# Optimization experiments

Measured on AMD Instinct MI355X. Metric: run time of the kernel, lower is better.

Reference implementation:

```python
import jax, jax.numpy as jnp
import numpy as np

EPS = 1e-5

def _conv1x1(x, w, b):
    # x: [B, Din, N], w: [Dout, Din], b: [Dout]
    return jnp.einsum('od,bdn->bon', w, x) + b[None, :, None]

def _layernorm_last(x):
    # LayerNorm over last axis, no affine (matches torch LayerNorm([N], elementwise_affine=False))
    mu = jnp.mean(x, axis=-1, keepdims=True)
    var = jnp.mean(jnp.square(x - mu), axis=-1, keepdims=True)
    return (x - mu) * jax.lax.rsqrt(var + EPS)

def setup_inputs() -> dict:
    key = jax.random.key(0)
    ks = jax.random.split(key, 16)
    B, D, N, M = 1, 64, 64 * 80, 4096
    H2 = 2 * D
    s = 0.05
    return {
        'fea_pixel': jax.random.normal(ks[0], (B, D, N), jnp.float32),
        'fea_keypoint': jax.random.normal(ks[1], (B, D, M), jnp.float32),
        'Wq': jax.random.normal(ks[2], (D, D), jnp.float32) * s,
        'bq': jax.random.normal(ks[3], (D,), jnp.float32) * s,
        'Wk': jax.random.normal(ks[4], (D, D), jnp.float32) * s,
        'bk': jax.random.normal(ks[5], (D,), jnp.float32) * s,
        'Wv': jax.random.normal(ks[6], (D, D), jnp.float32) * s,
        'bv': jax.random.normal(ks[7], (D,), jnp.float32) * s,
        'Wm': jax.random.normal(ks[8], (D, D), jnp.float32) * s,
        'bm': jax.random.normal(ks[9], (D,), jnp.float32) * s,
        'W1': jax.random.normal(ks[10], (H2, D), jnp.float32) * s,
        'b1': jax.random.normal(ks[11], (H2,), jnp.float32) * s,
        'W2': jax.random.normal(ks[12], (D, H2), jnp.float32) * s,
        'b2': jax.random.normal(ks[13], (D,), jnp.float32) * s,
    }

def reference(fea_pixel, fea_keypoint, Wq, bq, Wk, bk, Wv, bv, Wm, bm, W1, b1, W2, b2):
    B, D, N = fea_pixel.shape
    num_heads = 4
    hd = D // num_heads  # head dim

    # QKV 1x1-conv projections, then split channels as (head_dim, num_heads) -- matches torch view
    q = _conv1x1(fea_pixel, Wq, bq).reshape(B, hd, num_heads, N)
    k = _conv1x1(fea_keypoint, Wk, bk).reshape(B, hd, num_heads, -1)
    v = _conv1x1(fea_keypoint, Wv, bv).reshape(B, hd, num_heads, -1)

    scores = jnp.einsum('bdhn,bdhm->bhnm', q, k) / jnp.sqrt(jnp.float32(hd))
    prob = jax.nn.softmax(scores, axis=-1)
    x = jnp.einsum('bhnm,bdhm->bdhn', prob, v)  # [B, hd, H, N]
    attn = _conv1x1(x.reshape(B, D, N), Wm, bm)

    fea = _layernorm_last(fea_pixel + attn)  # [B, D, N]

    # MLP over channel dim: operate on [B, N, D]
    y = jnp.swapaxes(fea, 1, 2)
    h = jax.nn.relu(jnp.einsum('bnd,od->bno', y, W1) + b1)
    m = jax.nn.relu(jnp.einsum('bno,do->bnd', h, W2) + b2)

    return _layernorm_last(fea + jnp.swapaxes(m, 1, 2))
```

## Files before the change

### kernel.cpp

```cpp
#include <hip/hip_runtime.h>
#include <hip/hip_bf16.h>

typedef __attribute__((ext_vector_type(4))) short short4v;
typedef __attribute__((ext_vector_type(4))) float float4v;

#define NHEADS 4
#define DMODEL 64
#define EPSV 1e-5f
#define QSCALE 0.36067376022224085f

__device__ inline short bf16rn(float f) {
    __hip_bfloat16 h = __float2bfloat16(f);
    return __builtin_bit_cast(short, h);
}

__device__ inline float exp2fast(float x) { return __builtin_amdgcn_exp2f(x); }

__global__ __launch_bounds__(256)
void proj_all_k(const float* __restrict__ Wk, const float* __restrict__ bk,
                const float* __restrict__ Wv, const float* __restrict__ bv,
                const float* __restrict__ Wq, const float* __restrict__ bq,
                const float* __restrict__ fkey, const float* __restrict__ fpix,
                short4v* __restrict__ kfrag, short4v* __restrict__ vfrag,
                short4v* __restrict__ qfrag, int M, int N) {
    __shared__ float xs[64][64];
    __shared__ float wsm[64][65];
    const int t = threadIdx.x;
    const int kvblocks = M >> 6;
    const bool isKV = (int)blockIdx.x < kvblocks;
    const int c0 = (isKV ? blockIdx.x : blockIdx.x - kvblocks) * 64;
    const float* x = isKV ? fkey : fpix;
    const int NC = isKV ? M : N;

    for (int i = t; i < 64 * 64; i += 256) {
        xs[i >> 6][i & 63] = x[(size_t)(i >> 6) * NC + c0 + (i & 63)];
        if (isKV) wsm[i >> 6][i & 63] = Wv[i];
    }
    __syncthreads();
    const int CT = NC >> 4;

    {
        const float* W = isKV ? Wk : Wq;
        const float* b = isKV ? bk : bq;
        const float scale = isKV ? 1.f : QSCALE;
        short4v* outf = isKV ? kfrag : qfrag;
        const int mm = t & 63;
        const int qd = __builtin_amdgcn_readfirstlane(t >> 6);
        const int m = c0 + mm;
        float acc[16];
        #pragma unroll
        for (int cc = 0; cc < 16; ++cc) acc[cc] = b[qd * 16 + cc];
        #pragma unroll 8
        for (int d = 0; d < 64; ++d) {
            float xv = xs[d][mm];
            #pragma unroll
            for (int cc = 0; cc < 16; ++cc)
                acc[cc] = fmaf(W[(qd * 16 + cc) * 64 + d], xv, acc[cc]);
        }
        #pragma unroll
        for (int h = 0; h < 4; ++h) {
            short4v pk;
            #pragma unroll
            for (int j = 0; j < 4; ++j) pk[j] = bf16rn(acc[j * 4 + h] * scale);
            outf[((size_t)(h * CT + (m >> 4))) * 64 + (m & 15) + 16 * qd] = pk;
        }
    }
    if (isKV) {
        const int lane = t & 63;
        const int w = t >> 6;
        const int d = lane >> 2, h = lane & 3;
        const float b0 = bv[lane];
        #pragma unroll
        for (int r = 0; r < 4; ++r) {
            const int mg = r * 4 + w;
            float a0 = b0, a1 = b0, a2 = b0, a3 = b0;
            #pragma unroll 8
            for (int dd = 0; dd < 64; ++dd) {
                float wv = wsm[lane][dd];
                float4 xv = *(const float4*)&xs[dd][mg * 4];
                a0 = fmaf(wv, xv.x, a0); a1 = fmaf(wv, xv.y, a1);
                a2 = fmaf(wv, xv.z, a2); a3 = fmaf(wv, xv.w, a3);
            }
            short4v pk;
            pk[0] = bf16rn(a0); pk[1] = bf16rn(a1); pk[2] = bf16rn(a2); pk[3] = bf16rn(a3);
            const int m0 = c0 + mg * 4;
            vfrag[((size_t)(h * CT + (m0 >> 4))) * 64 + d + 16 * ((m0 >> 2) & 3)] = pk;
        }
    }
}

__global__ __launch_bounds__(256)
void attn_mfma_k(const short4v* __restrict__ qf, const short4v* __restrict__ kf,
                 const short4v* __restrict__ vf, float* __restrict__ xatt,
                 int N, int M) {
    const int lane = threadIdx.x & 63;
    const int ck = threadIdx.x >> 6;
    const int nt = blockIdx.x;
    const int h = blockIdx.y;
    const int NT = N >> 4, MT = M >> 4;
    const int mtN = MT >> 2;
    const int mt0 = ck * mtN;

    const short4v q4 = qf[((size_t)(h * NT + nt)) * 64 + lane];
    const float4v zero4 = {0.f, 0.f, 0.f, 0.f};
    float4v O = zero4;
    float ld = 0.f;
    const int g4 = (lane >> 4) << 2;

    const short4v* kp = kf + ((size_t)(h * MT + mt0)) * 64 + lane;
    const short4v* vp = vf + ((size_t)(h * MT + mt0)) * 64 + lane;
    for (int it = 0; it < mtN; it += 4) {
        short4v ka[4], va[4];
        #pragma unroll
        for (int u = 0; u < 4; ++u) {
            ka[u] = kp[(it + u) * 64];
            va[u] = vp[(it + u) * 64];
        }
        #pragma unroll
        for (int u = 0; u < 4; ++u) {
            float4v s = __builtin_amdgcn_mfma_f32_16x16x16bf16_1k(ka[u], q4, zero4, 0, 0, 0);
            float p0 = exp2fast(s[0]), p1 = exp2fast(s[1]),
                  p2 = exp2fast(s[2]), p3 = exp2fast(s[3]);
            ld += (p0 + p1) + (p2 + p3);
            short4v pa;
            pa[0] = bf16rn(p0); pa[1] = bf16rn(p1); pa[2] = bf16rn(p2); pa[3] = bf16rn(p3);
            O = __builtin_amdgcn_mfma_f32_16x16x16bf16_1k(pa, va[u], O, 0, 0, 0);
        }
    }
    ld += __shfl_xor(ld, 16);
    ld += __shfl_xor(ld, 32);

    __shared__ float Osm[4][256];
    __shared__ float lsm[4][16];
    #pragma unroll
    for (int b = 0; b < 4; ++b)
        Osm[ck][(g4 + b) * 16 + (lane & 15)] = O[b];
    if (lane < 16) lsm[ck][lane] = ld;
    __syncthreads();

    const int t = threadIdx.x;
    const int d = t >> 4, q = t & 15;
    const float L = (lsm[0][q] + lsm[1][q]) + (lsm[2][q] + lsm[3][q]);
    const int oi = q * 16 + d;
    const float val = (Osm[0][oi] + Osm[1][oi]) + (Osm[2][oi] + Osm[3][oi]);
    xatt[(size_t)(d * NHEADS + h) * N + nt * 16 + q] = val / L;
}

template<int DIN, int DOUT, bool RELU>
__global__ __launch_bounds__(256)
void conv1x1_k(const float* __restrict__ W, const float* __restrict__ bias,
               const float* __restrict__ x, float* __restrict__ out, int N) {
    __shared__ float xs[DIN][64];
    const int tid = threadIdx.x;
    const int n0 = blockIdx.x * 64;
    for (int i = tid; i < DIN * 64; i += 256) {
        int d = i >> 6, nn = i & 63;
        xs[d][nn] = x[(size_t)d * N + n0 + nn];
    }
    __syncthreads();
    const int nn = tid & 63;
    const int og = __builtin_amdgcn_readfirstlane((int)(threadIdx.x >> 6));
    const int ow = blockIdx.y * 16 + og * 4;
    float acc[4];
    #pragma unroll
    for (int i = 0; i < 4; ++i) acc[i] = bias[ow + i];
    #pragma unroll 8
    for (int d = 0; d < DIN; ++d) {
        float xv = xs[d][nn];
        #pragma unroll
        for (int i = 0; i < 4; ++i)
            acc[i] = fmaf(W[(ow + i) * DIN + d], xv, acc[i]);
    }
    #pragma unroll
    for (int i = 0; i < 4; ++i) {
        float r = RELU ? fmaxf(acc[i], 0.f) : acc[i];
        out[(size_t)(ow + i) * N + n0 + nn] = r;
    }
}

__global__ __launch_bounds__(512)
void add_ln_k(const float* __restrict__ a, const float* __restrict__ b,
              float* __restrict__ out, int N) {
    const int d = blockIdx.x;
    const int tid = threadIdx.x;
    const int nv = N >> 2;
    const float4* a4 = (const float4*)(a + (size_t)d * N);
    const float4* b4 = (const float4*)(b + (size_t)d * N);
    float4* o4 = (float4*)(out + (size_t)d * N);
    float s1 = 0.f, s2 = 0.f;
    for (int i = tid; i < nv; i += 512) {
        float4 va = a4[i], vb = b4[i];
        float tx = va.x + vb.x, ty = va.y + vb.y, tz = va.z + vb.z, tw = va.w + vb.w;
        s1 += (tx + ty) + (tz + tw);
        s2 = fmaf(tx, tx, s2); s2 = fmaf(ty, ty, s2);
        s2 = fmaf(tz, tz, s2); s2 = fmaf(tw, tw, s2);
    }
    #pragma unroll
    for (int m = 1; m < 64; m <<= 1) {
        s1 += __shfl_xor(s1, m);
        s2 += __shfl_xor(s2, m);
    }
    __shared__ float ws1[8], ws2[8];
    const int w = tid >> 6;
    if ((tid & 63) == 0) { ws1[w] = s1; ws2[w] = s2; }
    __syncthreads();
    s1 = 0.f; s2 = 0.f;
    #pragma unroll
    for (int i = 0; i < 8; ++i) { s1 += ws1[i]; s2 += ws2[i]; }
    const float mean = s1 / (float)N;
    const float var  = s2 / (float)N - mean * mean;
    const float rstd = rsqrtf(var + EPSV);
    for (int i = tid; i < nv; i += 512) {
        float4 va = a4[i], vb = b4[i];
        float4 r;
        r.x = (va.x + vb.x - mean) * rstd;
        r.y = (va.y + vb.y - mean) * rstd;
        r.z = (va.z + vb.z - mean) * rstd;
        r.w = (va.w + vb.w - mean) * rstd;
        o4[i] = r;
    }
}

extern "C" void kernel_launch(void* const* d_in, const int* in_sizes, int n_in,
                              void* d_out, int out_size, void* d_ws, size_t ws_size,
                              hipStream_t stream) {
    const float* fpix = (const float*)d_in[0];
    const float* fkey = (const float*)d_in[1];
    const float* Wq = (const float*)d_in[2];  const float* bq = (const float*)d_in[3];
    const float* Wk = (const float*)d_in[4];  const float* bk = (const float*)d_in[5];
    const float* Wv = (const float*)d_in[6];  const float* bv = (const float*)d_in[7];
    const float* Wm = (const float*)d_in[8];  const float* bm = (const float*)d_in[9];
    const float* W1 = (const float*)d_in[10]; const float* b1 = (const float*)d_in[11];
    const float* W2 = (const float*)d_in[12]; const float* b2 = (const float*)d_in[13];
    float* outp = (float*)d_out;

    const int N = in_sizes[0] / DMODEL;
    const int M = in_sizes[1] / DMODEL;

    char* wsb = (char*)d_ws;
    short4v* qfrag = (short4v*)(wsb);
    short4v* kfrag = (short4v*)(wsb + 655360);
    short4v* vfrag = (short4v*)(wsb + 1179648);
    float*   xatt  = (float*)(wsb + 1703936);
    float*   fea   = (float*)(wsb + 3014656);
    float*   attnb = (float*)(wsb + 4325376);
    float*   hbuf  = (float*)(wsb + 5636096);
    float*   mbuf  = (float*)(wsb + 8257536);

    proj_all_k<<<dim3(M / 64 + N / 64), 256, 0, stream>>>(Wk, bk, Wv, bv, Wq, bq,
                                                          fkey, fpix, kfrag, vfrag,
                                                          qfrag, M, N);
    attn_mfma_k<<<dim3(N / 16, NHEADS), 256, 0, stream>>>(qfrag, kfrag, vfrag, xatt, N, M);
    conv1x1_k<64, 64, false><<<dim3(N / 64, 4), 256, 0, stream>>>(Wm, bm, xatt, attnb, N);
    add_ln_k<<<64, 512, 0, stream>>>(fpix, attnb, fea, N);
    conv1x1_k<64, 128, true><<<dim3(N / 64, 8), 256, 0, stream>>>(W1, b1, fea, hbuf, N);
    conv1x1_k<128, 64, true><<<dim3(N / 64, 4), 256, 0, stream>>>(W2, b2, hbuf, mbuf, N);
    add_ln_k<<<64, 512, 0, stream>>>(fea, mbuf, outp, N);
}
```

Before: 66.65 us.

## Fuse residual+LN stats into conv epilogues and fuse MLP into one kernel

The Wm conv now adds the pixel residual and writes per-block partial sums and sums of squares for the first LayerNorm. A single fused MLP kernel finishes those statistics, normalizes on load, runs both matmuls through shared memory, adds the residual and emits partial stats for the second LayerNorm. A light finishing kernel then applies the final normalization. This removes the hidden-activation round trip through global memory and the two 64-block LayerNorm kernels, which had poor parallelism. In exchange, every block redundantly re-reduces the partial statistics, and the single-pass variance formula is less numerically stable.

```diff
diff --git a/kernel.cpp b/kernel.cpp
--- a/kernel.cpp
+++ b/kernel.cpp
@@ -146,78 +146,182 @@
     xatt[(size_t)(d * NHEADS + h) * N + nt * 16 + q] = val / L;
 }
 
-template<int DIN, int DOUT, bool RELU>
 __global__ __launch_bounds__(256)
-void conv1x1_k(const float* __restrict__ W, const float* __restrict__ bias,
-               const float* __restrict__ x, float* __restrict__ out, int N) {
-    __shared__ float xs[DIN][64];
+void conv_wm_resid_k(const float* __restrict__ W, const float* __restrict__ bias,
+                     const float* __restrict__ xatt, const float* __restrict__ fpix,
+                     float* __restrict__ resid, float* __restrict__ pb_s,
+                     float* __restrict__ pb_q, int N) {
+    __shared__ float xs[64][64];
     const int tid = threadIdx.x;
-    const int n0 = blockIdx.x * 64;
-    for (int i = tid; i < DIN * 64; i += 256) {
+    const int bx = blockIdx.x;
+    const int n0 = bx * 64;
+    for (int i = tid; i < 64 * 64; i += 256) {
         int d = i >> 6, nn = i & 63;
-        xs[d][nn] = x[(size_t)d * N + n0 + nn];
+        xs[d][nn] = xatt[(size_t)d * N + n0 + nn];
     }
     __syncthreads();
     const int nn = tid & 63;
-    const int og = __builtin_amdgcn_readfirstlane((int)(threadIdx.x >> 6));
+    const int og = __builtin_amdgcn_readfirstlane((int)(tid >> 6));
     const int ow = blockIdx.y * 16 + og * 4;
     float acc[4];
     #pragma unroll
     for (int i = 0; i < 4; ++i) acc[i] = bias[ow + i];
     #pragma unroll 8
-    for (int d = 0; d < DIN; ++d) {
+    for (int d = 0; d < 64; ++d) {
         float xv = xs[d][nn];
         #pragma unroll
         for (int i = 0; i < 4; ++i)
-            acc[i] = fmaf(W[(ow + i) * DIN + d], xv, acc[i]);
+            acc[i] = fmaf(W[(ow + i) * 64 + d], xv, acc[i]);
     }
     #pragma unroll
     for (int i = 0; i < 4; ++i) {
-        float r = RELU ? fmaxf(acc[i], 0.f) : acc[i];
-        out[(size_t)(ow + i) * N + n0 + nn] = r;
+        float r = acc[i] + fpix[(size_t)(ow + i) * N + n0 + nn];
+        resid[(size_t)(ow + i) * N + n0 + nn] = r;
+        float s = r, q = r * r;
+        #pragma unroll
+        for (int m = 1; m < 64; m <<= 1) {
+            s += __shfl_xor(s, m);
+            q += __shfl_xor(q, m);
+        }
+        if (nn == 0) {
+            pb_s[(ow + i) * (N >> 6) + bx] = s;
+            pb_q[(ow + i) * (N >> 6) + bx] = q;
+        }
     }
 }
 
 __global__ __launch_bounds__(512)
-void add_ln_k(const float* __restrict__ a, const float* __restrict__ b,
-              float* __restrict__ out, int N) {
-    const int d = blockIdx.x;
+void mlp_fused_k(const float* __restrict__ W1, const float* __restrict__ b1,
+                 const float* __restrict__ W2, const float* __restrict__ b2,
+                 const float* __restrict__ resid, const float* __restrict__ pb1s,
+                 const float* __restrict__ pb1q, float* __restrict__ tbuf,
+                 float* __restrict__ pb2s, float* __restrict__ pb2q, int N) {
+    __shared__ float xs[64][65];
+    __shared__ float hs[128][65];
+    __shared__ float redS[8][64], redQ[8][64];
+    __shared__ float lnA[64], lnB[64];
     const int tid = threadIdx.x;
-    const int nv = N >> 2;
-    const float4* a4 = (const float4*)(a + (size_t)d * N);
-    const float4* b4 = (const float4*)(b + (size_t)d * N);
-    float4* o4 = (float4*)(out + (size_t)d * N);
-    float s1 = 0.f, s2 = 0.f;
-    for (int i = tid; i < nv; i += 512) {
-        float4 va = a4[i], vb = b4[i];
-        float tx = va.x + vb.x, ty = va.y + vb.y, tz = va.z + vb.z, tw = va.w + vb.w;
-        s1 += (tx + ty) + (tz + tw);
-        s2 = fmaf(tx, tx, s2); s2 = fmaf(ty, ty, s2);
-        s2 = fmaf(tz, tz, s2); s2 = fmaf(tw, tw, s2);
-    }
+    const int nb = N >> 6;
+    const int bx = blockIdx.x;
+    const int n0 = bx * 64;
+
+    {
+        const int c = tid & 63, part = tid >> 6;
+        const int per = nb >> 3;
+        float s = 0.f, q = 0.f;
+        for (int i = 0; i < per; ++i) {
+            int b = part * per + i;
+            s += pb1s[c * nb + b];
+            q += pb1q[c * nb + b];
+        }
+        redS[part][c] = s; redQ[part][c] = q;
+    }
+    __syncthreads();
+    if (tid < 64) {
+        float s = 0.f, q = 0.f;
+        #pragma unroll
+        for (int p = 0; p < 8; ++p) { s += redS[p][tid]; q += redQ[p][tid]; }
+        float mean = s / (float)N;
+        float var = q / (float)N - mean * mean;
+        float rstd = rsqrtf(var + EPSV);
+        lnA[tid] = rstd;
+        lnB[tid] = -mean * rstd;
+    }
+    __syncthreads();
+
+    for (int i = tid; i < 64 * 64; i += 512) {
+        int c = i >> 6, nn = i & 63;
+        xs[c][nn] = resid[(size_t)c * N + n0 + nn] * lnA[c] + lnB[c];
+    }
+    __syncthreads();
+
+    const int col = tid & 63;
+    const int w = __builtin_amdgcn_readfirstlane((int)(tid >> 6));
+
     #pragma unroll
-    for (int m = 1; m < 64; m <<= 1) {
-        s1 += __shfl_xor(s1, m);
-        s2 += __shfl_xor(s2, m);
-    }
-    __shared__ float ws1[8], ws2[8];
-    const int w = tid >> 6;
-    if ((tid & 63) == 0) { ws1[w] = s1; ws2[w] = s2; }
-    __syncthreads();
-    s1 = 0.f; s2 = 0.f;
-    #pragma unroll
-    for (int i = 0; i < 8; ++i) { s1 += ws1[i]; s2 += ws2[i]; }
-    const float mean = s1 / (float)N;
-    const float var  = s2 / (float)N - mean * mean;
-    const float rstd = rsqrtf(var + EPSV);
-    for (int i = tid; i < nv; i += 512) {
-        float4 va = a4[i], vb = b4[i];
-        float4 r;
-        r.x = (va.x + vb.x - mean) * rstd;
-        r.y = (va.y + vb.y - mean) * rstd;
-        r.z = (va.z + vb.z - mean) * rstd;
-        r.w = (va.w + vb.w - mean) * rstd;
-        o4[i] = r;
+    for (int pass = 0; pass < 2; ++pass) {
+        const int h0 = w * 16 + pass * 8;
+        float acc[8];
+        #pragma unroll
+        for (int i = 0; i < 8; ++i) acc[i] = b1[h0 + i];
+        #pragma unroll 8
+        for (int c = 0; c < 64; ++c) {
+            float xv = xs[c][col];
+            #pragma unroll
+            for (int i = 0; i < 8; ++i)
+                acc[i] = fmaf(W1[(h0 + i) * 64 + c], xv, acc[i]);
+        }
+        #pragma unroll
+        for (int i = 0; i < 8; ++i)
+            hs[h0 + i][col] = fmaxf(acc[i], 0.f);
+    }
+    __syncthreads();
+
+    {
+        const int o0 = w * 8;
+        float acc[8];
+        #pragma unroll
+        for (int i = 0; i < 8; ++i) acc[i] = b2[o0 + i];
+        #pragma unroll 8
+        for (int c = 0; c < 128; ++c) {
+            float hv = hs[c][col];
+            #pragma unroll
+            for (int i = 0; i < 8; ++i)
+                acc[i] = fmaf(W2[(o0 + i) * 128 + c], hv, acc[i]);
+        }
+        #pragma unroll
+        for (int i = 0; i < 8; ++i) {
+            const int o = o0 + i;
+            float tv = xs[o][col] + fmaxf(acc[i], 0.f);
+            tbuf[(size_t)o * N + n0 + col] = tv;
+            float s = tv, q = tv * tv;
+            #pragma unroll
+            for (int m = 1; m < 64; m <<= 1) {
+                s += __shfl_xor(s, m);
+                q += __shfl_xor(q, m);
+            }
+            if (col == 0) {
+                pb2s[o * nb + bx] = s;
+                pb2q[o * nb + bx] = q;
+            }
+        }
+    }
+}
+
+__global__ __launch_bounds__(256)
+void ln_finish_k(const float* __restrict__ tbuf, const float* __restrict__ pb2s,
+                 const float* __restrict__ pb2q, float* __restrict__ out, int N) {
+    __shared__ float redS[4][64], redQ[4][64];
+    __shared__ float lnA[64], lnB[64];
+    const int tid = threadIdx.x;
+    const int nb = N >> 6;
+    {
+        const int c = tid & 63, part = tid >> 6;
+        const int per = nb >> 2;
+        float s = 0.f, q = 0.f;
+        for (int i = 0; i < per; ++i) {
+            int b = part * per + i;
+            s += pb2s[c * nb + b];
+            q += pb2q[c * nb + b];
+        }
+        redS[part][c] = s; redQ[part][c] = q;
+    }
+    __syncthreads();
+    if (tid < 64) {
+        float s = 0.f, q = 0.f;
+        #pragma unroll
+        for (int p = 0; p < 4; ++p) { s += redS[p][tid]; q += redQ[p][tid]; }
+        float mean = s / (float)N;
+        float var = q / (float)N - mean * mean;
+        float rstd = rsqrtf(var + EPSV);
+        lnA[tid] = rstd;
+        lnB[tid] = -mean * rstd;
+    }
+    __syncthreads();
+    const int n0 = blockIdx.x * 32;
+    for (int i = tid; i < 64 * 32; i += 256) {
+        int c = i >> 5, nn = i & 31;
+        out[(size_t)c * N + n0 + nn] = tbuf[(size_t)c * N + n0 + nn] * lnA[c] + lnB[c];
     }
 }
 
@@ -242,18 +346,20 @@
     short4v* kfrag = (short4v*)(wsb + 655360);
     short4v* vfrag = (short4v*)(wsb + 1179648);
     float*   xatt  = (float*)(wsb + 1703936);
-    float*   fea   = (float*)(wsb + 3014656);
-    float*   attnb = (float*)(wsb + 4325376);
-    float*   hbuf  = (float*)(wsb + 5636096);
-    float*   mbuf  = (float*)(wsb + 8257536);
+    float*   resid = (float*)(wsb + 3014656);
+    float*   tbuf  = (float*)(wsb + 4325376);
+    float*   pb1s  = (float*)(wsb + 5636096);
+    float*   pb1q  = (float*)(wsb + 5656576);
+    float*   pb2s  = (float*)(wsb + 5677056);
+    float*   pb2q  = (float*)(wsb + 5697536);
 
     proj_all_k<<<dim3(M / 64 + N / 64), 256, 0, stream>>>(Wk, bk, Wv, bv, Wq, bq,
                                                           fkey, fpix, kfrag, vfrag,
                                                           qfrag, M, N);
     attn_mfma_k<<<dim3(N / 16, NHEADS), 256, 0, stream>>>(qfrag, kfrag, vfrag, xatt, N, M);
-    conv1x1_k<64, 64, false><<<dim3(N / 64, 4), 256, 0, stream>>>(Wm, bm, xatt, attnb, N);
-    add_ln_k<<<64, 512, 0, stream>>>(fpix, attnb, fea, N);
-    conv1x1_k<64, 128, true><<<dim3(N / 64, 8), 256, 0, stream>>>(W1, b1, fea, hbuf, N);
-    conv1x1_k<128, 64, true><<<dim3(N / 64, 4), 256, 0, stream>>>(W2, b2, hbuf, mbuf, N);
-    add_ln_k<<<64, 512, 0, stream>>>(fea, mbuf, outp, N);
-}
+    conv_wm_resid_k<<<dim3(N / 64, 4), 256, 0, stream>>>(Wm, bm, xatt, fpix, resid,
+                                                         pb1s, pb1q, N);
+    mlp_fused_k<<<dim3(N / 64), 512, 0, stream>>>(W1, b1, W2, b2, resid,
+                                                  pb1s, pb1q, tbuf, pb2s, pb2q, N);
+    ln_finish_k<<<dim3(N / 32), 256, 0, stream>>>(tbuf, pb2s, pb2q, outp, N);
+}
```

Result: slower. 79.24 us (+18.9%).
